# Kernel tuning notes

Measured on AMD Instinct MI355X. Metric: run time of the kernel, lower is better.

Reference implementation:

```python
import jax, jax.numpy as jnp
import numpy as np
from jax import lax

G = 64       # grid_size
K = 8        # N_knn
L = 64       # latent size
NP = 150000  # num points
NEG_SLOPE = 0.01


def lrelu(x):
    return jnp.where(x >= 0, x, NEG_SLOPE * x)


def setup_inputs() -> dict:
    key = jax.random.key(0)
    ks = jax.random.split(key, 16)
    inp = {
        "pc_KNN_pos": jax.random.normal(ks[0], (NP, K, 3), jnp.float32),
        "points": jax.random.randint(ks[1], (NP, 3), 0, G),
        # point MLP: 3 -> 64 -> 64 (LeakyReLU between)
        "W1": jax.random.normal(ks[2], (3, L), jnp.float32) * 0.3,
        "b1": jnp.zeros((L,), jnp.float32),
        "W2": jax.random.normal(ks[3], (L, L), jnp.float32) * 0.1,
        "b2": jnp.zeros((L,), jnp.float32),
        # knn aggregator: Conv1d(K,K,1) -> LeakyReLU -> Conv1d(K,1,1)
        "Wk1": jax.random.normal(ks[4], (K, K), jnp.float32) * 0.3,
        "bk1": jnp.zeros((K,), jnp.float32),
        "Wk2": jax.random.normal(ks[5], (1, K), jnp.float32) * 0.3,
        "bk2": jnp.zeros((1,), jnp.float32),
        "Cw1": jax.random.normal(ks[6], (L, L, 3, 3, 3), jnp.float32) * 0.02,
        "Cb1": jnp.zeros((L,), jnp.float32),
        "Cw2": jax.random.normal(ks[7], (L, L, 3, 3, 3), jnp.float32) * 0.02,
        "Cb2": jnp.zeros((L,), jnp.float32),
    }
    return inp


def reference(pc_KNN_pos, points, W1, b1, W2, b2, Wk1, bk1, Wk2, bk2, Cw1, Cb1, Cw2, Cb2):
    # point MLP over last dim: (Np, K, 3) -> (Np, K, L)
    h = lrelu(pc_KNN_pos @ W1 + b1)
    feat = h @ W2 + b2
    # knn_feat: 1x1 Conv1d over channel dim K (spatial dim = L)
    f1 = lrelu(jnp.einsum('ok,nkl->nol', Wk1, feat) + bk1[None, :, None])
    f2 = jnp.einsum('ok,nkl->nol', Wk2, f1) + bk2[None, :, None]  # (Np, 1, L)
    pfeat = f2[:, 0, :]  # (Np, L)
    # AvgPooling: scatter-average point features into G^3 grid cells
    idx = (points[:, 0] * G + points[:, 1]) * G + points[:, 2]  # (Np,)
    sums = jax.ops.segment_sum(pfeat, idx, num_segments=G * G * G)
    cnt = jax.ops.segment_sum(jnp.ones((pfeat.shape[0], 1), pfeat.dtype), idx,
                              num_segments=G * G * G)
    grid = jnp.where(cnt > 0, sums / jnp.maximum(cnt, 1.0), 0.0)
    grid = grid.reshape(G, G, G, L)
    # grid convs: (G,G,G,L) -> (1,L,G,G,G) -> convs -> (G,G,G,L)
    x = grid.transpose(3, 0, 1, 2)[None]
    dn = ('NCDHW', 'OIDHW', 'NCDHW')
    for w, b in ((Cw1, Cb1), (Cw2, Cb2)):
        x = lax.conv_general_dilated(x, w, (1, 1, 1), [(1, 1)] * 3,
                                     dimension_numbers=dn)
        x = jax.nn.relu(x + b[None, :, None, None, None])
    return x[0].transpose(1, 2, 3, 0)  # (G,G,G,L)
```

## Files before the change

kernel.cpp:

```cpp
#include <hip/hip_runtime.h>
#include <hip/hip_fp16.h>

#define G 64
#define KNN 8

typedef _Float16 f16x2 __attribute__((ext_vector_type(2)));
typedef _Float16 f16x8 __attribute__((ext_vector_type(8)));
typedef float f32x16 __attribute__((ext_vector_type(16)));

static __device__ __forceinline__ f16x2 pkrtz(float a, float b) {
    return __builtin_bit_cast(f16x2, __builtin_amdgcn_cvt_pkrtz(a, b));
}
static __device__ __forceinline__ void plswap(f16x2& a, f16x2& b) {
    int ai = __builtin_bit_cast(int, a), bi = __builtin_bit_cast(int, b);
    asm("v_permlane32_swap_b32 %0, %1" : "+v"(ai), "+v"(bi));
    a = __builtin_bit_cast(f16x2, ai);
    b = __builtin_bit_cast(f16x2, bi);
}

__global__ __launch_bounds__(256) void point_mlp_scatter(
    const float* __restrict__ pos, const int* __restrict__ pts,
    const float* __restrict__ W1, const float* __restrict__ b1,
    const float* __restrict__ W2, const float* __restrict__ b2,
    const float* __restrict__ Wk1, const float* __restrict__ bk1,
    const float* __restrict__ Wk2, const float* __restrict__ bk2,
    float* __restrict__ sums, float* __restrict__ cnt, int np, int nslots)
{
    __shared__ _Float16 hb[4 * 2048];

    const int tid = threadIdx.x;
    const int wv = tid >> 6;
    const int l  = tid & 63;
    const int lr = l & 31;
    const int hi = l >> 5;

    int xp = hi, yp = 2 + hi;
    asm("v_permlane32_swap_b32 %0, %1" : "+v"(xp), "+v"(yp));
    const int chan = lr + ((xp & 2) ? 32 : 0);
    const int rot = (__builtin_amdgcn_readfirstlane(xp) != 0);

    const float w1r0 = W1[l], w1r1 = W1[64 + l], w1r2 = W1[128 + l];
    const float b1v = b1[l];
    const float b2v0 = b2[lr], b2v1 = b2[32 + lr];

    f16x8 bfr[2][4];
    #pragma unroll
    for (int nf = 0; nf < 2; ++nf)
        #pragma unroll
        for (int ks = 0; ks < 4; ++ks) {
            f16x8 v;
            #pragma unroll
            for (int i = 0; i < 8; ++i)
                v[i] = (_Float16)W2[(ks * 16 + hi * 8 + i) * 64 + nf * 32 + lr];
            bfr[nf][ks] = v;
        }

    f16x2 wk1p[32];
    float bk1v[8];
    #pragma unroll
    for (int o = 0; o < 8; ++o) {
        #pragma unroll
        for (int j = 0; j < 4; ++j)
            wk1p[o * 4 + j] = f16x2{(_Float16)Wk1[o * 8 + 2 * j],
                                    (_Float16)Wk1[o * 8 + 2 * j + 1]};
        bk1v[o] = bk1[o];
    }
    f16x2 wk2p[4];
    #pragma unroll
    for (int j = 0; j < 4; ++j)
        wk2p[j] = f16x2{(_Float16)Wk2[2 * j], (_Float16)Wk2[2 * j + 1]};
    const float bk2v = bk2[0];

    _Float16* hw = hb + wv * 2048;
    const int r7 = lr & 7;

    const int ngrp = (np + 3) >> 2;
    for (int g = blockIdx.x * 4 + wv; g < ngrp; g += nslots) {
        const int gu = __builtin_amdgcn_readfirstlane(g);
        const int p0 = gu * 4;

        #pragma unroll
        for (int pl = 0; pl < 4; ++pl) {
            const float* pp = pos + (size_t)((p0 + pl < np) ? (p0 + pl) : (np - 1)) * 24;
            #pragma unroll
            for (int kk = 0; kk < KNN; ++kk) {
                const int row = pl * 8 + kk;
                float x0 = pp[kk * 3 + 0], x1 = pp[kk * 3 + 1], x2 = pp[kk * 3 + 2];
                float h = fmaf(x2, w1r2, fmaf(x1, w1r1, fmaf(x0, w1r0, b1v)));
                h = fmaxf(h, 0.01f * h);
                hw[row * 64 + (l ^ ((row & 7) << 3))] = (_Float16)h;
            }
        }

        f16x8 a[4];
        #pragma unroll
        for (int ks = 0; ks < 4; ++ks)
            a[ks] = *(const f16x8*)&hw[lr * 64 + (((ks * 2 + hi) ^ r7) << 3)];

        f32x16 acc0, acc1;
        #pragma unroll
        for (int q = 0; q < 16; ++q) { acc0[q] = 0.f; acc1[q] = 0.f; }
        #pragma unroll
        for (int ks = 0; ks < 4; ++ks) {
            acc0 = __builtin_amdgcn_mfma_f32_32x32x16_f16(a[ks], bfr[0][ks], acc0, 0, 0, 0);
            acc1 = __builtin_amdgcn_mfma_f32_32x32x16_f16(a[ks], bfr[1][ks], acc1, 0, 0, 0);
        }
        #pragma unroll
        for (int q = 0; q < 16; ++q) { acc0[q] += b2v0; acc1[q] += b2v1; }

        float pfv[4];
        #pragma unroll
        for (int pl = 0; pl < 4; ++pl) {
            f16x2 x1 = pkrtz(acc0[pl * 4 + 0], acc0[pl * 4 + 1]);
            f16x2 x2 = pkrtz(acc0[pl * 4 + 2], acc0[pl * 4 + 3]);
            f16x2 y1 = pkrtz(acc1[pl * 4 + 0], acc1[pl * 4 + 1]);
            f16x2 y2 = pkrtz(acc1[pl * 4 + 2], acc1[pl * 4 + 3]);
            plswap(x1, y1);
            plswap(x2, y2);
            f16x2 k01 = rot ? y1 : x1;
            f16x2 k23 = rot ? y2 : x2;
            f16x2 k45 = rot ? x1 : y1;
            f16x2 k67 = rot ? x2 : y2;
            float f1[8];
            #pragma unroll
            for (int o = 0; o < 8; ++o) {
                float f = bk1v[o];
                f = __builtin_amdgcn_fdot2(k01, wk1p[o * 4 + 0], f, false);
                f = __builtin_amdgcn_fdot2(k23, wk1p[o * 4 + 1], f, false);
                f = __builtin_amdgcn_fdot2(k45, wk1p[o * 4 + 2], f, false);
                f = __builtin_amdgcn_fdot2(k67, wk1p[o * 4 + 3], f, false);
                f1[o] = fmaxf(f, 0.01f * f);
            }
            float pf = bk2v;
            #pragma unroll
            for (int j = 0; j < 4; ++j)
                pf = __builtin_amdgcn_fdot2(pkrtz(f1[2 * j], f1[2 * j + 1]), wk2p[j], pf, false);
            pfv[pl] = pf;
        }

        const int* pq = pts + (size_t)p0 * 3;
        #pragma unroll
        for (int pl = 0; pl < 4; ++pl) {
            if (p0 + pl < np) {
                int cell = (pq[pl * 3 + 0] * G + pq[pl * 3 + 1]) * G + pq[pl * 3 + 2];
                atomicAdd(&sums[(size_t)cell * 64 + chan], pfv[pl]);
                if (l == 0) atomicAdd(&cnt[cell], 1.0f);
            }
        }
    }
}

__global__ __launch_bounds__(256) void convert_dense(
    const float* __restrict__ sums, const float* __restrict__ cnt,
    _Float16* __restrict__ g16)
{
    int cb = blockIdx.x;
    int cb2 = (cb & 7) * 1024 + (cb >> 3);
    int t = cb2 * 256 + threadIdx.x;
    int cell = t >> 3, slot = t & 7;
    float c = cnt[cell];
    float inv = (c > 0.f) ? 1.f / c : 0.f;
    const float4* p = (const float4*)&sums[(size_t)cell * 64 + slot * 8];
    float4 a = p[0], b = p[1];
    f16x8 v = f16x8{(_Float16)(a.x * inv), (_Float16)(a.y * inv),
                    (_Float16)(a.z * inv), (_Float16)(a.w * inv),
                    (_Float16)(b.x * inv), (_Float16)(b.y * inv),
                    (_Float16)(b.z * inv), (_Float16)(b.w * inv)};
    *(f16x8*)&g16[(size_t)cell * 64 + slot * 8] = v;
}

__global__ __launch_bounds__(256) void transform_w_fp16(
    const float* __restrict__ w, _Float16* __restrict__ wT)
{
    int o = blockIdx.x * 256 + threadIdx.x;
    if (o < 27 * 4 * 2 * 64 * 8) {
        int i   = o & 7;
        int l   = (o >> 3) & 63;
        int nf  = (o >> 9) & 1;
        int ks  = (o >> 10) & 3;
        int tap = o >> 12;
        int co = nf * 32 + (l & 31);
        int ci = ks * 16 + (l >> 5) * 8 + i;
        wT[o] = (_Float16)w[(co * 64 + ci) * 27 + tap];
    }
}

template<int OUT_F32>
__global__ __launch_bounds__(256, 3) void conv3d_z4(
    const _Float16* __restrict__ in, const _Float16* __restrict__ wT,
    const float* __restrict__ bias, void* __restrict__ out_)
{
    __shared__ ushort tile[600 * 32];

    const int lb = blockIdx.x;
    const int bx = (lb & 7) * 128 + (lb >> 3);
    const int X0 = (bx & 7) * 8, Y0 = ((bx >> 3) & 7) * 8, Z0 = (bx >> 6) * 4;
    const int tid = threadIdx.x;
    const int lane = tid & 63;
    const int wv   = tid >> 6;
    const int lr   = lane & 31;
    const int hi   = lane >> 5;

    int base_m[2];
    #pragma unroll
    for (int mt = 0; mt < 2; ++mt)
        base_m[mt] = wv * 100 + (mt * 4 + (lr >> 3)) * 10 + (lr & 7);

    f32x16 acc[2][2];
    #pragma unroll
    for (int mt = 0; mt < 2; ++mt)
        #pragma unroll
        for (int nf = 0; nf < 2; ++nf)
            #pragma unroll
            for (int q = 0; q < 16; ++q) acc[mt][nf][q] = 0.f;

    const f16x8* wTB = (const f16x8*)wT;

    uint4 h1r[10];
    #pragma unroll
    for (int n = 0; n < 10; ++n) {
        const int c = n * 256 + tid;
        if (c < 2400) {
            const int vox = c >> 2, t = c & 3;
            const int hz = vox / 100, r0 = vox - hz * 100;
            const int hy = r0 / 10, hx = r0 - hy * 10;
            const int gz = Z0 + hz - 1, gy = Y0 + hy - 1, gx = X0 + hx - 1;
            const bool ok = ((unsigned)gz < 64u) && ((unsigned)gy < 64u) && ((unsigned)gx < 64u);
            uint4 v0 = make_uint4(0u, 0u, 0u, 0u);
            uint4 v1 = make_uint4(0u, 0u, 0u, 0u);
            if (ok) {
                const ushort* q = (const ushort*)in +
                    ((size_t)((gz * 64 + gy) * 64 + gx) * 64 + t * 8);
                v0 = *(const uint4*)q;
                v1 = *(const uint4*)(q + 32);
            }
            const int dst = vox * 32 + ((((vox >> 1) + t) & 3) << 3);
            *(uint4*)&tile[dst] = v0;
            h1r[n] = v1;
        }
    }
    __syncthreads();

    auto kloop = [&](int half) {
        #pragma unroll
        for (int dz = 0; dz < 3; ++dz)
        #pragma unroll
        for (int dy = 0; dy < 3; ++dy)
        #pragma unroll
        for (int dx = 0; dx < 3; ++dx) {
            const int tap = (dz * 3 + dy) * 3 + dx;
            const int rowoff = dz * 100 + dy * 10 + dx;
            const f16x8* wB = wTB + tap * 512 + lane;
            f16x8 B0[2], B1[2];
            #pragma unroll
            for (int ksp = 0; ksp < 2; ++ksp) {
                const int ks = half * 2 + ksp;
                B0[ksp] = wB[(ks * 2 + 0) * 64];
                B1[ksp] = wB[(ks * 2 + 1) * 64];
            }
            #pragma unroll
            for (int ksp = 0; ksp < 2; ++ksp) {
                const int c8 = ksp * 2 + hi;
                #pragma unroll
                for (int mt = 0; mt < 2; ++mt) {
                    const int voxr = base_m[mt] + rowoff;
                    f16x8 a = *(const f16x8*)&tile[voxr * 32 + ((((voxr >> 1) + c8) & 3) << 3)];
                    acc[mt][0] = __builtin_amdgcn_mfma_f32_32x32x16_f16(a, B0[ksp], acc[mt][0], 0, 0, 0);
                    acc[mt][1] = __builtin_amdgcn_mfma_f32_32x32x16_f16(a, B1[ksp], acc[mt][1], 0, 0, 0);
                }
            }
        }
    };

    kloop(0);
    __syncthreads();

    #pragma unroll
    for (int n = 0; n < 10; ++n) {
        const int c = n * 256 + tid;
        if (c < 2400) {
            const int vox = c >> 2, t = c & 3;
            const int dst = vox * 32 + ((((vox >> 1) + t) & 3) << 3);
            *(uint4*)&tile[dst] = h1r[n];
        }
    }
    __syncthreads();

    kloop(1);

    const float bv0 = bias[lr], bv1 = bias[32 + lr];
    #pragma unroll
    for (int mt = 0; mt < 2; ++mt) {
        #pragma unroll
        for (int r = 0; r < 16; ++r) {
            int row = (r & 3) + 8 * (r >> 2) + 4 * hi;
            int vlw = mt * 32 + row;
            int gy = Y0 + (vlw >> 3), gx = X0 + (vlw & 7), gz = Z0 + wv;
            size_t off = (((size_t)(gz * 64 + gy) * 64 + gx) << 6) + lr;
            float v0 = fmaxf(acc[mt][0][r] + bv0, 0.f);
            float v1 = fmaxf(acc[mt][1][r] + bv1, 0.f);
            if (OUT_F32) {
                ((float*)out_)[off]      = v0;
                ((float*)out_)[off + 32] = v1;
            } else {
                ((_Float16*)out_)[off]      = (_Float16)v0;
                ((_Float16*)out_)[off + 32] = (_Float16)v1;
            }
        }
    }
}

extern "C" void kernel_launch(void* const* d_in, const int* in_sizes, int n_in,
                              void* d_out, int out_size, void* d_ws, size_t ws_size,
                              hipStream_t stream)
{
    const float* pos  = (const float*)d_in[0];
    const int*   pts  = (const int*)  d_in[1];
    const float* W1   = (const float*)d_in[2];
    const float* b1   = (const float*)d_in[3];
    const float* W2   = (const float*)d_in[4];
    const float* b2   = (const float*)d_in[5];
    const float* Wk1  = (const float*)d_in[6];
    const float* bk1  = (const float*)d_in[7];
    const float* Wk2  = (const float*)d_in[8];
    const float* bk2  = (const float*)d_in[9];
    const float* Cw1  = (const float*)d_in[10];
    const float* Cb1  = (const float*)d_in[11];
    const float* Cw2  = (const float*)d_in[12];
    const float* Cb2  = (const float*)d_in[13];

    float* out = (float*)d_out;
    char*  ws  = (char*)d_ws;
    _Float16* g16  = (_Float16*)ws;
    _Float16* c1d  = (_Float16*)(ws + 33554432);
    float*    cntb = (float*)(ws + 67108864);
    _Float16* wT1  = (_Float16*)(ws + 68157440);
    _Float16* wT2  = (_Float16*)(ws + 68378624);

    const int np = in_sizes[0] / 24;

    (void)hipMemsetAsync(out,  0, 67108864, stream);
    (void)hipMemsetAsync(cntb, 0, 1048576, stream);

    transform_w_fp16<<<432, 256, 0, stream>>>(Cw1, wT1);
    transform_w_fp16<<<432, 256, 0, stream>>>(Cw2, wT2);

    const int nblk = 2048;
    point_mlp_scatter<<<nblk, 256, 0, stream>>>(
        pos, pts, W1, b1, W2, b2, Wk1, bk1, Wk2, bk2, out, cntb, np, nblk * 4);

    convert_dense<<<8192, 256, 0, stream>>>(out, cntb, g16);

    conv3d_z4<0><<<1024, 256, 0, stream>>>(g16, wT1, Cb1, (void*)c1d);
    conv3d_z4<1><<<1024, 256, 0, stream>>>(c1d, wT2, Cb2, (void*)out);
}
```

Measured before the change: 315.2 us.

## Process two z-slabs per conv block with software-pipelined halo loads

Each conv3d block now handles an 8-deep z range as two 4-deep slabs. Global loads for the next channel half or slab are issued before the current MFMA loop, so memory latency overlaps compute, and the grid shrinks to 512 blocks. Occupancy hint drops from 3 to 2 blocks per CU to leave registers for the double buffers, and the LDS swizzle is simplified. The risks are lower occupancy and fewer blocks for load balance across CUs.

```diff
diff --git a/kernel.cpp b/kernel.cpp
--- a/kernel.cpp
+++ b/kernel.cpp
@@ -186,15 +186,15 @@
 }
 
 template<int OUT_F32>
-__global__ __launch_bounds__(256, 3) void conv3d_z4(
+__global__ __launch_bounds__(256, 2) void conv3d_pipe(
     const _Float16* __restrict__ in, const _Float16* __restrict__ wT,
     const float* __restrict__ bias, void* __restrict__ out_)
 {
     __shared__ ushort tile[600 * 32];
 
     const int lb = blockIdx.x;
-    const int bx = (lb & 7) * 128 + (lb >> 3);
-    const int X0 = (bx & 7) * 8, Y0 = ((bx >> 3) & 7) * 8, Z0 = (bx >> 6) * 4;
+    const int bx = (lb & 7) * 64 + (lb >> 3);
+    const int X0 = (bx & 7) * 8, Y0 = ((bx >> 3) & 7) * 8, Zb = (bx >> 6) * 8;
     const int tid = threadIdx.x;
     const int lane = tid & 63;
     const int wv   = tid >> 6;
@@ -215,32 +215,35 @@
             for (int q = 0; q < 16; ++q) acc[mt][nf][q] = 0.f;
 
     const f16x8* wTB = (const f16x8*)wT;
-
-    uint4 h1r[10];
-    #pragma unroll
-    for (int n = 0; n < 10; ++n) {
-        const int c = n * 256 + tid;
-        if (c < 2400) {
-            const int vox = c >> 2, t = c & 3;
-            const int hz = vox / 100, r0 = vox - hz * 100;
-            const int hy = r0 / 10, hx = r0 - hy * 10;
-            const int gz = Z0 + hz - 1, gy = Y0 + hy - 1, gx = X0 + hx - 1;
-            const bool ok = ((unsigned)gz < 64u) && ((unsigned)gy < 64u) && ((unsigned)gx < 64u);
-            uint4 v0 = make_uint4(0u, 0u, 0u, 0u);
-            uint4 v1 = make_uint4(0u, 0u, 0u, 0u);
-            if (ok) {
-                const ushort* q = (const ushort*)in +
-                    ((size_t)((gz * 64 + gy) * 64 + gx) * 64 + t * 8);
-                v0 = *(const uint4*)q;
-                v1 = *(const uint4*)(q + 32);
-            }
-            const int dst = vox * 32 + ((((vox >> 1) + t) & 3) << 3);
-            *(uint4*)&tile[dst] = v0;
-            h1r[n] = v1;
-        }
-    }
-    __syncthreads();
-
+    const float bv0 = bias[lr], bv1 = bias[32 + lr];
+
+    auto issue = [&](uint4 (&arr)[10], int Z0, int half) {
+        #pragma unroll
+        for (int n = 0; n < 10; ++n) {
+            const int c = n * 256 + tid;
+            uint4 v = make_uint4(0u, 0u, 0u, 0u);
+            if (c < 2400) {
+                const int vox = c >> 2, t = c & 3;
+                const int hz = vox / 100, r0 = vox - hz * 100;
+                const int hy = r0 / 10, hx = r0 - hy * 10;
+                const int gz = Z0 + hz - 1, gy = Y0 + hy - 1, gx = X0 + hx - 1;
+                if (((unsigned)gz < 64u) && ((unsigned)gy < 64u) && ((unsigned)gx < 64u))
+                    v = *(const uint4*)(in +
+                        ((size_t)((gz * 64 + gy) * 64 + gx) * 64 + half * 32 + t * 8));
+            }
+            arr[n] = v;
+        }
+    };
+    auto commit = [&](uint4 (&arr)[10]) {
+        #pragma unroll
+        for (int n = 0; n < 10; ++n) {
+            const int c = n * 256 + tid;
+            if (c < 2400) {
+                const int vox = c >> 2, t = c & 3;
+                *(uint4*)&tile[vox * 32 + (((t + vox) & 3) << 3)] = arr[n];
+            }
+        }
+    };
     auto kloop = [&](int half) {
         #pragma unroll
         for (int dz = 0; dz < 3; ++dz)
@@ -264,50 +267,61 @@
                 #pragma unroll
                 for (int mt = 0; mt < 2; ++mt) {
                     const int voxr = base_m[mt] + rowoff;
-                    f16x8 a = *(const f16x8*)&tile[voxr * 32 + ((((voxr >> 1) + c8) & 3) << 3)];
+                    f16x8 a = *(const f16x8*)&tile[voxr * 32 + (((c8 + voxr) & 3) << 3)];
                     acc[mt][0] = __builtin_amdgcn_mfma_f32_32x32x16_f16(a, B0[ksp], acc[mt][0], 0, 0, 0);
                     acc[mt][1] = __builtin_amdgcn_mfma_f32_32x32x16_f16(a, B1[ksp], acc[mt][1], 0, 0, 0);
                 }
             }
         }
     };
-
+    auto epilogue = [&](int Z0) {
+        #pragma unroll
+        for (int mt = 0; mt < 2; ++mt) {
+            #pragma unroll
+            for (int r = 0; r < 16; ++r) {
+                int row = (r & 3) + 8 * (r >> 2) + 4 * hi;
+                int vlw = mt * 32 + row;
+                int gy = Y0 + (vlw >> 3), gx = X0 + (vlw & 7), gz = Z0 + wv;
+                size_t off = (((size_t)(gz * 64 + gy) * 64 + gx) << 6) + lr;
+                float v0 = fmaxf(acc[mt][0][r] + bv0, 0.f);
+                float v1 = fmaxf(acc[mt][1][r] + bv1, 0.f);
+                if (OUT_F32) {
+                    ((float*)out_)[off]      = v0;
+                    ((float*)out_)[off + 32] = v1;
+                } else {
+                    ((_Float16*)out_)[off]      = (_Float16)v0;
+                    ((_Float16*)out_)[off + 32] = (_Float16)v1;
+                }
+                acc[mt][0][r] = 0.f;
+                acc[mt][1][r] = 0.f;
+            }
+        }
+    };
+
+    uint4 A[10], B[10];
+
+    issue(A, Zb, 0);
+    commit(A);
+    __syncthreads();
+    issue(B, Zb, 1);
     kloop(0);
     __syncthreads();
-
-    #pragma unroll
-    for (int n = 0; n < 10; ++n) {
-        const int c = n * 256 + tid;
-        if (c < 2400) {
-            const int vox = c >> 2, t = c & 3;
-            const int dst = vox * 32 + ((((vox >> 1) + t) & 3) << 3);
-            *(uint4*)&tile[dst] = h1r[n];
-        }
-    }
-    __syncthreads();
-
+    commit(B);
+    __syncthreads();
+    issue(A, Zb + 4, 0);
     kloop(1);
-
-    const float bv0 = bias[lr], bv1 = bias[32 + lr];
-    #pragma unroll
-    for (int mt = 0; mt < 2; ++mt) {
-        #pragma unroll
-        for (int r = 0; r < 16; ++r) {
-            int row = (r & 3) + 8 * (r >> 2) + 4 * hi;
-            int vlw = mt * 32 + row;
-            int gy = Y0 + (vlw >> 3), gx = X0 + (vlw & 7), gz = Z0 + wv;
-            size_t off = (((size_t)(gz * 64 + gy) * 64 + gx) << 6) + lr;
-            float v0 = fmaxf(acc[mt][0][r] + bv0, 0.f);
-            float v1 = fmaxf(acc[mt][1][r] + bv1, 0.f);
-            if (OUT_F32) {
-                ((float*)out_)[off]      = v0;
-                ((float*)out_)[off + 32] = v1;
-            } else {
-                ((_Float16*)out_)[off]      = (_Float16)v0;
-                ((_Float16*)out_)[off + 32] = (_Float16)v1;
-            }
-        }
-    }
+    epilogue(Zb);
+
+    __syncthreads();
+    commit(A);
+    __syncthreads();
+    issue(B, Zb + 4, 1);
+    kloop(0);
+    __syncthreads();
+    commit(B);
+    __syncthreads();
+    kloop(1);
+    epilogue(Zb + 4);
 }
 
 extern "C" void kernel_launch(void* const* d_in, const int* in_sizes, int n_in,
@@ -351,6 +365,6 @@
 
     convert_dense<<<8192, 256, 0, stream>>>(out, cntb, g16);
 
-    conv3d_z4<0><<<1024, 256, 0, stream>>>(g16, wT1, Cb1, (void*)c1d);
-    conv3d_z4<1><<<1024, 256, 0, stream>>>(c1d, wT2, Cb2, (void*)out);
-}
+    conv3d_pipe<0><<<512, 256, 0, stream>>>(g16, wT1, Cb1, (void*)c1d);
+    conv3d_pipe<1><<<512, 256, 0, stream>>>(c1d, wT2, Cb2, (void*)out);
+}
```

After: 341.2 us. +8.2%, slower.
